# Kernel optimization log

Measured on AMD Instinct MI355X. Metric: run time of the kernel, lower is better.

## Reference

```python
import math
import jax, jax.numpy as jnp
import numpy as np

B, L, D, H = 4, 2048, 512, 8
DK = D // H  # d_keys = d_values = 64
KFAC = 3


def setup_inputs() -> dict:
    key = jax.random.key(0)
    ks = jax.random.split(key, 10)
    u_part = min(KFAC * int(math.ceil(math.log(L))), L)  # 24
    scale = 1.0 / math.sqrt(D)
    return {
        "queries": jax.random.normal(ks[0], (B, L, D), jnp.float32),
        "keys": jax.random.normal(ks[1], (B, L, D), jnp.float32),
        "values": jax.random.normal(ks[2], (B, L, D), jnp.float32),
        "index_sample": jax.random.randint(ks[3], (L, u_part), 0, L, jnp.int32),
        "Wq": jax.random.normal(ks[4], (D, D), jnp.float32) * scale,
        "bq": jnp.zeros((D,), jnp.float32),
        "Wk": jax.random.normal(ks[5], (D, D), jnp.float32) * scale,
        "bk": jnp.zeros((D,), jnp.float32),
        "Wv": jax.random.normal(ks[6], (D, D), jnp.float32) * scale,
        "bv": jnp.zeros((D,), jnp.float32),
        "Wo": jax.random.normal(ks[7], (D, D), jnp.float32) * scale,
        "bo": jnp.zeros((D,), jnp.float32),
    }


def reference(queries, keys, values, index_sample, Wq, bq, Wk, bk, Wv, bv, Wo, bo):
    b, q_len, d_out = queries.shape
    k_len = keys.shape[1]
    # projections -> [B, H, L, DK]
    q = (queries @ Wq + bq).reshape(b, q_len, H, DK).transpose(0, 2, 1, 3)
    k = (keys @ Wk + bk).reshape(b, k_len, H, DK).transpose(0, 2, 1, 3)
    v = (values @ Wv + bv).reshape(b, k_len, H, DK).transpose(0, 2, 1, 3)

    n_top = min(KFAC * int(math.ceil(math.log(q_len))), q_len)  # u

    # --- _prob_qk: sampled QK scores to pick sparse queries ---
    # k_sample: [B, H, q_len, sample_k, DK]
    k_sample = k[:, :, index_sample, :]
    q_k_sample = jnp.einsum("bhld,bhlsd->bhls", q, k_sample)
    m = jnp.max(q_k_sample, axis=-1) - jnp.sum(q_k_sample, axis=-1) / k_len
    _, m_top = jax.lax.top_k(m, n_top)  # [B, H, u]

    q_reduce = jnp.take_along_axis(q, m_top[..., None], axis=2)  # [B, H, u, DK]
    scores_top = jnp.einsum("bhud,bhkd->bhuk", q_reduce, k) / math.sqrt(d_out)

    # --- masked (causal) branch: mask_flag=True ---
    causal = jnp.triu(jnp.ones((q_len, k_len), bool), 1)
    indicator = causal[m_top]  # [B, H, u, k_len]
    scores_top = jnp.where(indicator, -jnp.inf, scores_top)

    attn = jax.nn.softmax(scores_top, axis=-1)  # [B, H, u, k_len]
    context = jnp.cumsum(v, axis=2)  # default context for non-selected queries
    attn_values = jnp.einsum("bhuk,bhkd->bhud", attn, v)

    bidx = jnp.arange(b)[:, None, None]
    hidx = jnp.arange(H)[None, :, None]
    context = context.at[bidx, hidx, m_top].set(attn_values)

    # mix=False: transpose back to [B, L, H, DV] then merge heads
    context = context.transpose(0, 2, 1, 3).reshape(b, q_len, H * DK)
    out = context @ Wo + bo  # dropout_rate=0 / inference: identity
    return out
```

## Files before the change

### kernel.cpp

```cpp
#include <hip/hip_runtime.h>
#include <hip/hip_bf16.h>
#include <math.h>

#define Bq 4
#define Lq 2048
#define Dq 512
#define Hq 8
#define DKq 64
#define Uq 24
#define TSCAN 16
#define NTILE (Lq / TSCAN)
#define JCH 256
#define NCH (Lq / JCH)
#define TKCH 8
#define PAD 40

typedef unsigned short ushort_t;
typedef unsigned long long u64;
typedef __attribute__((ext_vector_type(8))) short bfrag8;
typedef __attribute__((ext_vector_type(4))) float facc4;

__device__ inline ushort_t bf16_rne(float f) {
  unsigned u = __float_as_uint(f);
  u += 0x7FFF + ((u >> 16) & 1);
  return (ushort_t)(u >> 16);
}
__device__ inline float bf16f(ushort_t h) {
  return __uint_as_float(((unsigned)h) << 16);
}
__device__ inline unsigned fkey(float f) {
  unsigned u = __float_as_uint(f);
  return (u & 0x80000000u) ? ~u : (u | 0x80000000u);
}

__global__ __launch_bounds__(256) void transpose_cast4(
    const float* __restrict__ W0, const float* __restrict__ W1,
    const float* __restrict__ W2, const float* __restrict__ W3,
    ushort_t* __restrict__ T0h, ushort_t* __restrict__ T0l,
    ushort_t* __restrict__ T1h, ushort_t* __restrict__ T1l,
    ushort_t* __restrict__ T2h, ushort_t* __restrict__ T3h) {
  __shared__ float tile[32][33];
  int z = blockIdx.z;
  const float* W = z == 0 ? W0 : (z == 1 ? W1 : (z == 2 ? W2 : W3));
  ushort_t* Th = z == 0 ? T0h : (z == 1 ? T1h : (z == 2 ? T2h : T3h));
  ushort_t* Tl = z == 0 ? T0l : (z == 1 ? T1l : nullptr);
  int k0 = blockIdx.x * 32, n0 = blockIdx.y * 32;
  int tx = threadIdx.x & 31, ty = threadIdx.x >> 5;
  for (int r = ty; r < 32; r += 8)
    tile[tx][r] = W[(size_t)(k0 + r) * 512 + n0 + tx];
  __syncthreads();
  for (int r = ty; r < 32; r += 8) {
    float v = tile[r][tx];
    ushort_t h = bf16_rne(v);
    Th[(size_t)(n0 + r) * 512 + k0 + tx] = h;
    if (Tl) Tl[(size_t)(n0 + r) * 512 + k0 + tx] = bf16_rne(v - bf16f(h));
  }
}

__global__ __launch_bounds__(256) void gemm_qkv(
    const float* __restrict__ Xq, const float* __restrict__ Xk,
    const float* __restrict__ Xv,
    const ushort_t* __restrict__ Wqh, const ushort_t* __restrict__ Wql,
    const ushort_t* __restrict__ Wkh, const ushort_t* __restrict__ Wkl,
    const ushort_t* __restrict__ Wvh,
    const float* __restrict__ bq, const float* __restrict__ bk,
    const float* __restrict__ bv,
    float* __restrict__ qo, float* __restrict__ ko, float* __restrict__ vo) {
  __shared__ ushort_t Ash[128][PAD], Asl[128][PAD];
  __shared__ ushort_t Bsh[128][PAD], Bsl[128][PAD];
  int which = blockIdx.z;
  const float* A = which == 0 ? Xq : (which == 1 ? Xk : Xv);
  const ushort_t* Bh = which == 0 ? Wqh : (which == 1 ? Wkh : Wvh);
  const ushort_t* Bl = which == 0 ? Wql : Wkl;
  const float* bias = which == 0 ? bq : (which == 1 ? bk : bv);
  float* C = which == 0 ? qo : (which == 1 ? ko : vo);
  const bool split = which < 2;

  int bm = blockIdx.x, bn = blockIdx.y;
  int tid = threadIdx.x;
  int wave = tid >> 6, lane = tid & 63;
  int wm = (wave & 1) * 64, wn = (wave >> 1) * 64;
  int quad = lane >> 4, lm = lane & 15;
  facc4 acc[4][4] = {};

  for (int k0 = 0; k0 < 512; k0 += 32) {
#pragma unroll
    for (int p = 0; p < 2; ++p) {
      int s = p * 256 + tid;
      int row = s >> 2, kq = (s & 3) * 8;
      const float* src = &A[(size_t)(bm * 128 + row) * 512 + k0 + kq];
      float4 x0 = *(const float4*)src;
      float4 x1 = *(const float4*)(src + 4);
      float xs[8] = {x0.x, x0.y, x0.z, x0.w, x1.x, x1.y, x1.z, x1.w};
      bfrag8 hv;
#pragma unroll
      for (int e = 0; e < 8; ++e) hv[e] = (short)bf16_rne(xs[e]);
      *(bfrag8*)&Ash[row][kq] = hv;
      if (split) {
        bfrag8 lv;
#pragma unroll
        for (int e = 0; e < 8; ++e)
          lv[e] = (short)bf16_rne(xs[e] - bf16f((ushort_t)hv[e]));
        *(bfrag8*)&Asl[row][kq] = lv;
      }
    }
#pragma unroll
    for (int p = 0; p < 2; ++p) {
      int s = p * 256 + tid;
      int row = s >> 2, kq = (s & 3) * 8;
      size_t g = (size_t)(bn * 128 + row) * 512 + k0 + kq;
      *(bfrag8*)&Bsh[row][kq] = *(const bfrag8*)&Bh[g];
      if (split) *(bfrag8*)&Bsl[row][kq] = *(const bfrag8*)&Bl[g];
    }
    __syncthreads();
    bfrag8 afh[4], afl[4], bfh[4], bfl[4];
#pragma unroll
    for (int mt = 0; mt < 4; ++mt) {
      afh[mt] = *(bfrag8*)&Ash[wm + mt * 16 + lm][quad * 8];
      if (split) afl[mt] = *(bfrag8*)&Asl[wm + mt * 16 + lm][quad * 8];
    }
#pragma unroll
    for (int nt = 0; nt < 4; ++nt) {
      bfh[nt] = *(bfrag8*)&Bsh[wn + nt * 16 + lm][quad * 8];
      if (split) bfl[nt] = *(bfrag8*)&Bsl[wn + nt * 16 + lm][quad * 8];
    }
#pragma unroll
    for (int mt = 0; mt < 4; ++mt)
#pragma unroll
      for (int nt = 0; nt < 4; ++nt) {
        facc4 a = acc[mt][nt];
        a = __builtin_amdgcn_mfma_f32_16x16x32_bf16(afh[mt], bfh[nt], a, 0, 0, 0);
        if (split) {
          a = __builtin_amdgcn_mfma_f32_16x16x32_bf16(afl[mt], bfh[nt], a, 0, 0, 0);
          a = __builtin_amdgcn_mfma_f32_16x16x32_bf16(afh[mt], bfl[nt], a, 0, 0, 0);
        }
        acc[mt][nt] = a;
      }
    __syncthreads();
  }
#pragma unroll
  for (int mt = 0; mt < 4; ++mt)
#pragma unroll
    for (int nt = 0; nt < 4; ++nt) {
      int col = bn * 128 + wn + nt * 16 + lm;
      float bv2 = bias[col];
#pragma unroll
      for (int r = 0; r < 4; ++r) {
        int row = bm * 128 + wm + mt * 16 + quad * 4 + r;
        C[(size_t)row * 512 + col] = acc[mt][nt][r] + bv2;
      }
    }
}

__global__ __launch_bounds__(256) void gemm_bf16(
    const ushort_t* __restrict__ A, const ushort_t* __restrict__ Bt,
    const float* __restrict__ bias, float* __restrict__ C) {
  __shared__ ushort_t As[128][PAD];
  __shared__ ushort_t Bs[128][PAD];
  int bm = blockIdx.x, bn = blockIdx.y;
  int tid = threadIdx.x;
  int wave = tid >> 6, lane = tid & 63;
  int wm = (wave & 1) * 64, wn = (wave >> 1) * 64;
  int quad = lane >> 4, lm = lane & 15;
  facc4 acc[4][4] = {};

  for (int k0 = 0; k0 < 512; k0 += 32) {
#pragma unroll
    for (int p = 0; p < 2; ++p) {
      int s = p * 256 + tid;
      int row = s >> 2, kq = (s & 3) * 8;
      *(bfrag8*)&As[row][kq] =
          *(const bfrag8*)&A[(size_t)(bm * 128 + row) * 512 + k0 + kq];
      *(bfrag8*)&Bs[row][kq] =
          *(const bfrag8*)&Bt[(size_t)(bn * 128 + row) * 512 + k0 + kq];
    }
    __syncthreads();
    bfrag8 af[4], bf[4];
#pragma unroll
    for (int mt = 0; mt < 4; ++mt)
      af[mt] = *(bfrag8*)&As[wm + mt * 16 + lm][quad * 8];
#pragma unroll
    for (int nt = 0; nt < 4; ++nt)
      bf[nt] = *(bfrag8*)&Bs[wn + nt * 16 + lm][quad * 8];
#pragma unroll
    for (int mt = 0; mt < 4; ++mt)
#pragma unroll
      for (int nt = 0; nt < 4; ++nt)
        acc[mt][nt] = __builtin_amdgcn_mfma_f32_16x16x32_bf16(
            af[mt], bf[nt], acc[mt][nt], 0, 0, 0);
    __syncthreads();
  }
#pragma unroll
  for (int mt = 0; mt < 4; ++mt)
#pragma unroll
    for (int nt = 0; nt < 4; ++nt) {
      int col = bn * 128 + wn + nt * 16 + lm;
      float bv = bias[col];
#pragma unroll
      for (int r = 0; r < 4; ++r) {
        int row = bm * 128 + wm + mt * 16 + quad * 4 + r;
        C[(size_t)row * 512 + col] = acc[mt][nt][r] + bv;
      }
    }
}

__global__ __launch_bounds__(256) void compute_m(
    const float* __restrict__ q, const float* __restrict__ k,
    const int* __restrict__ idxs, float* __restrict__ m) {
  int wave = threadIdx.x >> 6, lane = threadIdx.x & 63;
  int lq = lane >> 4, dq = lane & 15;
  int slot = (blockIdx.x * 4 + wave) * 4 + lq;
  int l = slot & (Lq - 1);
  int bh = slot >> 11;
  int h = bh & (Hq - 1), b = bh >> 3;
  float4 qv = *(const float4*)&q[((size_t)b * Lq + l) * Dq + h * DKq + dq * 4];
  const float* kb = &k[(size_t)b * Lq * Dq + h * DKq + dq * 4];
  const int* ib = &idxs[l * Uq];
  float mx = -INFINITY, sm = 0.f;
#pragma unroll
  for (int s = 0; s < Uq; ++s) {
    int j = ib[s];
    float4 kv = *(const float4*)&kb[(size_t)j * Dq];
    float p = qv.x * kv.x + qv.y * kv.y + qv.z * kv.z + qv.w * kv.w;
    p += __shfl_xor(p, 1, 64);
    p += __shfl_xor(p, 2, 64);
    p += __shfl_xor(p, 4, 64);
    p += __shfl_xor(p, 8, 64);
    mx = fmaxf(mx, p);
    sm += p;
  }
  if (dq == 0) m[slot] = mx - sm * (1.0f / Lq);
}

__device__ inline void bitonic256_desc(u64* s, int tid) {
  for (int k = 2; k <= 256; k <<= 1) {
    for (int j = k >> 1; j > 0; j >>= 1) {
      int p = tid ^ j;
      u64 mine = s[tid], other = s[p];
      u64 mx = mine > other ? mine : other;
      u64 mn = mine > other ? other : mine;
      bool dir = (tid & k) == 0;
      bool lower = tid < p;
      u64 res = dir ? (lower ? mx : mn) : (lower ? mn : mx);
      __syncthreads();
      s[tid] = res;
      __syncthreads();
    }
  }
}

__global__ __launch_bounds__(256) void topk_stage1(
    const float* __restrict__ m, u64* __restrict__ cand) {
  __shared__ u64 s[256];
  int bh = blockIdx.x >> 3;
  int ch = blockIdx.x & 7;
  int tid = threadIdx.x;
  int gidx = ch * 256 + tid;
  float v = m[(size_t)bh * Lq + gidx];
  s[tid] = ((u64)fkey(v) << 32) | (u64)(Lq - 1 - gidx);
  __syncthreads();
  bitonic256_desc(s, tid);
  if (tid < Uq) cand[((size_t)bh * TKCH + ch) * Uq + tid] = s[tid];
}

__global__ __launch_bounds__(256) void topk_stage2(
    const u64* __restrict__ cand, int* __restrict__ mtop) {
  __shared__ u64 s[256];
  int bh = blockIdx.x;
  int tid = threadIdx.x;
  s[tid] = (tid < TKCH * Uq) ? cand[(size_t)bh * TKCH * Uq + tid] : 0ull;
  __syncthreads();
  bitonic256_desc(s, tid);
  if (tid < Uq) mtop[bh * Uq + tid] = Lq - 1 - (int)(s[tid] & 0xFFFFFFFFull);
}

__global__ __launch_bounds__(256) void make_repl(
    const int* __restrict__ mtop, int* __restrict__ repl) {
  __shared__ int mt[Uq];
  int bh = blockIdx.x >> 3;
  int ch = blockIdx.x & 7;
  int tid = threadIdx.x;
  if (tid < Uq) mt[tid] = mtop[bh * Uq + tid];
  __syncthreads();
  int l = ch * 256 + tid;
  int u = -1;
#pragma unroll
  for (int s = 0; s < Uq; ++s)
    if (mt[s] == l) u = s;
  repl[(size_t)bh * Lq + l] = u;
}

#define JT 256
#define JS 64

__global__ __launch_bounds__(256) void scores_kernel(
    const float* __restrict__ q, const float* __restrict__ k,
    const int* __restrict__ mtop, float* __restrict__ scg) {
  __shared__ float qs[Uq][DKq + 1];
  __shared__ float ks[JS][DKq + 1];
  __shared__ int i0s[Uq];
  int bh = blockIdx.y;
  int jt = blockIdx.x;
  int h = bh & (Hq - 1);
  int b = bh >> 3;
  int tid = threadIdx.x;
  if (tid < Uq) i0s[tid] = mtop[bh * Uq + tid];
  __syncthreads();
  for (int s = tid; s < Uq * 16; s += 256) {
    int u = s >> 4, qd = (s & 15) * 4;
    float4 t = *(const float4*)&q[((size_t)b * Lq + i0s[u]) * Dq + h * DKq + qd];
    qs[u][qd] = t.x; qs[u][qd + 1] = t.y; qs[u][qd + 2] = t.z; qs[u][qd + 3] = t.w;
  }
  int jp = tid & 31;
  int ug = tid >> 5;
  const float scale = 0.044194173824159216f;
  for (int sub = 0; sub < JT / JS; ++sub) {
    int jbase = jt * JT + sub * JS;
    __syncthreads();
    for (int s = tid; s < JS * 16; s += 256) {
      int j = s >> 4, qd = (s & 15) * 4;
      float4 t = *(const float4*)&k[((size_t)b * Lq + jbase + j) * Dq + h * DKq + qd];
      ks[j][qd] = t.x; ks[j][qd + 1] = t.y; ks[j][qd + 2] = t.z; ks[j][qd + 3] = t.w;
    }
    __syncthreads();
    float acc[3][2] = {};
    int j0 = jp * 2, j1 = j0 + 1;
#pragma unroll 8
    for (int d = 0; d < DKq; ++d) {
      float k0 = ks[j0][d], k1 = ks[j1][d];
#pragma unroll
      for (int uu = 0; uu < 3; ++uu) {
        float qv = qs[ug * 3 + uu][d];
        acc[uu][0] += qv * k0;
        acc[uu][1] += qv * k1;
      }
    }
#pragma unroll
    for (int uu = 0; uu < 3; ++uu) {
      int u = ug * 3 + uu;
      scg[((size_t)(bh * Uq + u)) * Lq + jbase + j0] = acc[uu][0] * scale;
      scg[((size_t)(bh * Uq + u)) * Lq + jbase + j1] = acc[uu][1] * scale;
    }
  }
}

__global__ __launch_bounds__(256) void softmax_pv_partial(
    const float* __restrict__ scg, const float* __restrict__ v,
    const int* __restrict__ mtop, float* __restrict__ pmax,
    float* __restrict__ psum, float* __restrict__ pvp) {
  int blk = blockIdx.y;
  int jc = blockIdx.x;
  int bh = blk / Uq;
  int h = bh & (Hq - 1);
  int b = bh >> 3;
  int n = mtop[blk] + 1;
  int j0 = jc * JCH;
  if (j0 >= n) return;
  int cnt = min(JCH, n - j0);
  int tid = threadIdx.x, wave = tid >> 6, lane = tid & 63;
  __shared__ float es[JCH];
  __shared__ float red[4][DKq];
  __shared__ float rr[4];

  const float* row = &scg[(size_t)blk * Lq + j0];
  float mx = (tid < cnt) ? row[tid] : -INFINITY;
#pragma unroll
  for (int off = 32; off; off >>= 1) mx = fmaxf(mx, __shfl_xor(mx, off, 64));
  if (lane == 0) rr[wave] = mx;
  __syncthreads();
  mx = fmaxf(fmaxf(rr[0], rr[1]), fmaxf(rr[2], rr[3]));
  __syncthreads();

  float e = (tid < cnt) ? __expf(row[tid] - mx) : 0.f;
  es[tid] = e;
  float sm = e;
#pragma unroll
  for (int off = 32; off; off >>= 1) sm += __shfl_xor(sm, off, 64);
  if (lane == 0) rr[wave] = sm;
  __syncthreads();

  float acc = 0.f;
  const float* vb = &v[((size_t)b * Lq + j0) * Dq + h * DKq + lane];
  int jlo = wave * 64;
  int jhi = min(jlo + 64, cnt);
#pragma unroll 4
  for (int j = jlo; j < jhi; ++j) acc += es[j] * vb[(size_t)j * Dq];
  red[wave][lane] = acc;
  __syncthreads();
  if (wave == 0) {
    if (lane == 0) {
      pmax[blk * NCH + jc] = mx;
      psum[blk * NCH + jc] = rr[0] + rr[1] + rr[2] + rr[3];
    }
    pvp[((size_t)blk * NCH + jc) * DKq + lane] =
        red[0][lane] + red[1][lane] + red[2][lane] + red[3][lane];
  }
}

__global__ __launch_bounds__(256) void softmax_pv_combine(
    const float* __restrict__ pmax, const float* __restrict__ psum,
    const float* __restrict__ pvp, const int* __restrict__ mtop,
    float* __restrict__ attnv) {
  int blk = blockIdx.x * 4 + (threadIdx.x >> 6);
  int lane = threadIdx.x & 63;
  int n = mtop[blk] + 1;
  int nc = (n + JCH - 1) / JCH;
  float gmax = -INFINITY;
  for (int c = 0; c < nc; ++c) gmax = fmaxf(gmax, pmax[blk * NCH + c]);
  float tot = 0.f, acc = 0.f;
  for (int c = 0; c < nc; ++c) {
    float w = __expf(pmax[blk * NCH + c] - gmax);
    tot += psum[blk * NCH + c] * w;
    acc += pvp[((size_t)blk * NCH + c) * DKq + lane] * w;
  }
  attnv[(size_t)blk * DKq + lane] = acc / tot;
}

__global__ __launch_bounds__(128) void tile_sum(const float* __restrict__ v,
                                                float* __restrict__ tsum) {
  int blk = blockIdx.x;
  int tile = blk & (NTILE - 1);
  int b = blk >> 7;
  int d4 = threadIdx.x;
  float4 s = {0.f, 0.f, 0.f, 0.f};
  const float* base = &v[((size_t)b * Lq + tile * TSCAN) * Dq + d4 * 4];
#pragma unroll
  for (int r = 0; r < TSCAN; ++r) {
    float4 x = *(const float4*)&base[(size_t)r * Dq];
    s.x += x.x; s.y += x.y; s.z += x.z; s.w += x.w;
  }
  *(float4*)&tsum[((size_t)b * NTILE + tile) * Dq + d4 * 4] = s;
}

__global__ __launch_bounds__(128) void build_context(
    const float* __restrict__ v, const float* __restrict__ tsum,
    const int* __restrict__ repl, const float* __restrict__ attnv,
    ushort_t* __restrict__ ctxh) {
  int blk = blockIdx.x;
  int tile = blk & (NTILE - 1);
  int b = blk >> 7;
  int d4 = threadIdx.x;
  int h = d4 >> 4;
  float4 run = {0.f, 0.f, 0.f, 0.f};
  const float* tb = &tsum[(size_t)b * NTILE * Dq + d4 * 4];
  for (int i = 0; i < tile; ++i) {
    float4 t = *(const float4*)&tb[(size_t)i * Dq];
    run.x += t.x; run.y += t.y; run.z += t.z; run.w += t.w;
  }
  const int* replb = &repl[(size_t)(b * Hq + h) * Lq + tile * TSCAN];
  const float* vb = &v[((size_t)b * Lq + tile * TSCAN) * Dq + d4 * 4];
  ushort_t* cb = &ctxh[((size_t)b * Lq + tile * TSCAN) * Dq + d4 * 4];
  const float* ab = &attnv[(size_t)(b * Hq + h) * Uq * DKq + (d4 & 15) * 4];
#pragma unroll
  for (int r = 0; r < TSCAN; ++r) {
    float4 x = *(const float4*)&vb[(size_t)r * Dq];
    run.x += x.x; run.y += x.y; run.z += x.z; run.w += x.w;
    int u = replb[r];
    float4 val = run;
    if (u >= 0) val = *(const float4*)&ab[(size_t)u * DKq];
    ushort4 o = {bf16_rne(val.x), bf16_rne(val.y), bf16_rne(val.z),
                 bf16_rne(val.w)};
    *(ushort4*)&cb[(size_t)r * Dq] = o;
  }
}

extern "C" void kernel_launch(void* const* d_in, const int* in_sizes, int n_in,
                              void* d_out, int out_size, void* d_ws,
                              size_t ws_size, hipStream_t stream) {
  const float* queries = (const float*)d_in[0];
  const float* keys    = (const float*)d_in[1];
  const float* values  = (const float*)d_in[2];
  const int*   idxs    = (const int*)d_in[3];
  const float* Wq = (const float*)d_in[4];
  const float* bq = (const float*)d_in[5];
  const float* Wk = (const float*)d_in[6];
  const float* bk = (const float*)d_in[7];
  const float* Wv = (const float*)d_in[8];
  const float* bv = (const float*)d_in[9];
  const float* Wo = (const float*)d_in[10];
  const float* bo = (const float*)d_in[11];
  float* out = (float*)d_out;

  const size_t BLD = (size_t)Bq * Lq * Dq;
  char* w = (char*)d_ws;
  float* q    = (float*)w; w += BLD * 4;
  float* k    = (float*)w; w += BLD * 4;
  float* v    = (float*)w; w += BLD * 4;
  float* scg  = (float*)w; w += (size_t)Bq * Hq * Uq * Lq * 4;
  float* m    = (float*)w; w += (size_t)Bq * Hq * Lq * 4;
  float* attnv= (float*)w; w += (size_t)Bq * Hq * Uq * DKq * 4;
  float* tsum = (float*)w; w += (size_t)Bq * NTILE * Dq * 4;
  int* mtop   = (int*)w;   w += Bq * Hq * Uq * 4;
  int* repl   = (int*)w;   w += (size_t)Bq * Hq * Lq * 4;
  float* pmax = (float*)w; w += (size_t)Bq * Hq * Uq * NCH * 4;
  float* psum = (float*)w; w += (size_t)Bq * Hq * Uq * NCH * 4;
  float* pvp  = (float*)w; w += (size_t)Bq * Hq * Uq * NCH * DKq * 4;
  u64* cand   = (u64*)w;   w += (size_t)Bq * Hq * TKCH * Uq * 8;
  ushort_t* ctxh = (ushort_t*)w; w += BLD * 2;
  const size_t WSZ = 512 * 512;
  ushort_t* Wqh = (ushort_t*)w; w += WSZ * 2;
  ushort_t* Wql = (ushort_t*)w; w += WSZ * 2;
  ushort_t* Wkh = (ushort_t*)w; w += WSZ * 2;
  ushort_t* Wkl = (ushort_t*)w; w += WSZ * 2;
  ushort_t* Wvh = (ushort_t*)w; w += WSZ * 2;
  ushort_t* Woh = (ushort_t*)w; w += WSZ * 2;

  {
    dim3 tgrid(16, 16, 4);
    transpose_cast4<<<tgrid, 256, 0, stream>>>(Wq, Wk, Wv, Wo, Wqh, Wql, Wkh,
                                               Wkl, Wvh, Woh);
  }

  {
    dim3 ggrid(64, 4, 3);
    gemm_qkv<<<ggrid, 256, 0, stream>>>(queries, keys, values, Wqh, Wql, Wkh,
                                        Wkl, Wvh, bq, bk, bv, q, k, v);
  }

  compute_m<<<(Bq * Hq * Lq) / 16, 256, 0, stream>>>(q, k, idxs, m);
  topk_stage1<<<Bq * Hq * TKCH, 256, 0, stream>>>(m, cand);
  topk_stage2<<<Bq * Hq, 256, 0, stream>>>(cand, mtop);
  make_repl<<<Bq * Hq * 8, 256, 0, stream>>>(mtop, repl);

  {
    dim3 sgrid(Lq / JT, Bq * Hq);
    scores_kernel<<<sgrid, 256, 0, stream>>>(q, k, mtop, scg);
  }
  {
    dim3 pgrid(NCH, Bq * Hq * Uq);
    softmax_pv_partial<<<pgrid, 256, 0, stream>>>(scg, v, mtop, pmax, psum, pvp);
    softmax_pv_combine<<<Bq * Hq * Uq / 4, 256, 0, stream>>>(pmax, psum, pvp,
                                                             mtop, attnv);
  }

  tile_sum<<<Bq * NTILE, 128, 0, stream>>>(v, tsum);
  build_context<<<Bq * NTILE, 128, 0, stream>>>(v, tsum, repl, attnv, ctxh);

  {
    dim3 ggrid(64, 4);
    gemm_bf16<<<ggrid, 256, 0, stream>>>(ctxh, Woh, bo, out);
  }
}
```

Before: 302.4 us.

## Pre-cast activations to bf16 hi/lo and load GEMM tiles via global_load_lds

Adds separate cast kernels that split the fp32 query/key/value inputs into bf16 hi (and lo) arrays ahead of time, so the QKV GEMM no longer converts inside its main loop. Both GEMMs now stage A/B tiles with direct global-to-LDS 16-byte loads and drop the LDS row padding. This is meant to cut per-tile VALU conversion and register round-trips in the GEMM loops. In exchange it adds three extra kernel launches and an extra full read/write pass over the activations. Unpadded LDS rows may also cause bank conflicts on the fragment reads.

```diff
diff --git a/kernel.cpp b/kernel.cpp
--- a/kernel.cpp
+++ b/kernel.cpp
@@ -13,7 +13,6 @@
 #define JCH 256
 #define NCH (Lq / JCH)
 #define TKCH 8
-#define PAD 40
 
 typedef unsigned short ushort_t;
 typedef unsigned long long u64;
@@ -31,6 +30,35 @@
 __device__ inline unsigned fkey(float f) {
   unsigned u = __float_as_uint(f);
   return (u & 0x80000000u) ? ~u : (u | 0x80000000u);
+}
+__device__ __forceinline__ void gl2lds16(const void* g, void* l) {
+  __builtin_amdgcn_global_load_lds(
+      (const __attribute__((address_space(1))) unsigned*)g,
+      (__attribute__((address_space(3))) unsigned*)l, 16, 0, 0);
+}
+
+__global__ __launch_bounds__(256) void cast_hilo(
+    const float* __restrict__ x, ushort_t* __restrict__ hi,
+    ushort_t* __restrict__ lo, int n4) {
+  int t = blockIdx.x * 256 + threadIdx.x;
+  if (t >= n4) return;
+  float4 v = *(const float4*)&x[(size_t)t * 4];
+  ushort_t h0 = bf16_rne(v.x), h1 = bf16_rne(v.y), h2 = bf16_rne(v.z),
+           h3 = bf16_rne(v.w);
+  ushort4 hh = {h0, h1, h2, h3};
+  ushort4 ll = {bf16_rne(v.x - bf16f(h0)), bf16_rne(v.y - bf16f(h1)),
+                bf16_rne(v.z - bf16f(h2)), bf16_rne(v.w - bf16f(h3))};
+  *(ushort4*)&hi[(size_t)t * 4] = hh;
+  *(ushort4*)&lo[(size_t)t * 4] = ll;
+}
+
+__global__ __launch_bounds__(256) void cast_hi(
+    const float* __restrict__ x, ushort_t* __restrict__ hi, int n4) {
+  int t = blockIdx.x * 256 + threadIdx.x;
+  if (t >= n4) return;
+  float4 v = *(const float4*)&x[(size_t)t * 4];
+  ushort4 hh = {bf16_rne(v.x), bf16_rne(v.y), bf16_rne(v.z), bf16_rne(v.w)};
+  *(ushort4*)&hi[(size_t)t * 4] = hh;
 }
 
 __global__ __launch_bounds__(256) void transpose_cast4(
@@ -58,18 +86,20 @@
 }
 
 __global__ __launch_bounds__(256) void gemm_qkv(
-    const float* __restrict__ Xq, const float* __restrict__ Xk,
-    const float* __restrict__ Xv,
+    const ushort_t* __restrict__ Aqh, const ushort_t* __restrict__ Aql,
+    const ushort_t* __restrict__ Akh, const ushort_t* __restrict__ Akl,
+    const ushort_t* __restrict__ Avh,
     const ushort_t* __restrict__ Wqh, const ushort_t* __restrict__ Wql,
     const ushort_t* __restrict__ Wkh, const ushort_t* __restrict__ Wkl,
     const ushort_t* __restrict__ Wvh,
     const float* __restrict__ bq, const float* __restrict__ bk,
     const float* __restrict__ bv,
     float* __restrict__ qo, float* __restrict__ ko, float* __restrict__ vo) {
-  __shared__ ushort_t Ash[128][PAD], Asl[128][PAD];
-  __shared__ ushort_t Bsh[128][PAD], Bsl[128][PAD];
+  __shared__ ushort_t Ash[128][32], Asl[128][32];
+  __shared__ ushort_t Bsh[128][32], Bsl[128][32];
   int which = blockIdx.z;
-  const float* A = which == 0 ? Xq : (which == 1 ? Xk : Xv);
+  const ushort_t* Ah = which == 0 ? Aqh : (which == 1 ? Akh : Avh);
+  const ushort_t* Al = which == 0 ? Aql : Akl;
   const ushort_t* Bh = which == 0 ? Wqh : (which == 1 ? Wkh : Wvh);
   const ushort_t* Bl = which == 0 ? Wql : Wkl;
   const float* bias = which == 0 ? bq : (which == 1 ? bk : bv);
@@ -81,36 +111,21 @@
   int wave = tid >> 6, lane = tid & 63;
   int wm = (wave & 1) * 64, wn = (wave >> 1) * 64;
   int quad = lane >> 4, lm = lane & 15;
+  int srow = tid >> 2, skq = (tid & 3) * 8;
   facc4 acc[4][4] = {};
 
   for (int k0 = 0; k0 < 512; k0 += 32) {
 #pragma unroll
     for (int p = 0; p < 2; ++p) {
-      int s = p * 256 + tid;
-      int row = s >> 2, kq = (s & 3) * 8;
-      const float* src = &A[(size_t)(bm * 128 + row) * 512 + k0 + kq];
-      float4 x0 = *(const float4*)src;
-      float4 x1 = *(const float4*)(src + 4);
-      float xs[8] = {x0.x, x0.y, x0.z, x0.w, x1.x, x1.y, x1.z, x1.w};
-      bfrag8 hv;
-#pragma unroll
-      for (int e = 0; e < 8; ++e) hv[e] = (short)bf16_rne(xs[e]);
-      *(bfrag8*)&Ash[row][kq] = hv;
+      int row = srow + p * 64;
+      size_t ga = (size_t)(bm * 128 + row) * 512 + k0 + skq;
+      size_t gb = (size_t)(bn * 128 + row) * 512 + k0 + skq;
+      gl2lds16(&Ah[ga], &Ash[row][skq]);
+      gl2lds16(&Bh[gb], &Bsh[row][skq]);
       if (split) {
-        bfrag8 lv;
-#pragma unroll
-        for (int e = 0; e < 8; ++e)
-          lv[e] = (short)bf16_rne(xs[e] - bf16f((ushort_t)hv[e]));
-        *(bfrag8*)&Asl[row][kq] = lv;
+        gl2lds16(&Al[ga], &Asl[row][skq]);
+        gl2lds16(&Bl[gb], &Bsl[row][skq]);
       }
-    }
-#pragma unroll
-    for (int p = 0; p < 2; ++p) {
-      int s = p * 256 + tid;
-      int row = s >> 2, kq = (s & 3) * 8;
-      size_t g = (size_t)(bn * 128 + row) * 512 + k0 + kq;
-      *(bfrag8*)&Bsh[row][kq] = *(const bfrag8*)&Bh[g];
-      if (split) *(bfrag8*)&Bsl[row][kq] = *(const bfrag8*)&Bl[g];
     }
     __syncthreads();
     bfrag8 afh[4], afl[4], bfh[4], bfl[4];
@@ -155,24 +170,22 @@
 __global__ __launch_bounds__(256) void gemm_bf16(
     const ushort_t* __restrict__ A, const ushort_t* __restrict__ Bt,
     const float* __restrict__ bias, float* __restrict__ C) {
-  __shared__ ushort_t As[128][PAD];
-  __shared__ ushort_t Bs[128][PAD];
+  __shared__ ushort_t As[128][32];
+  __shared__ ushort_t Bs[128][32];
   int bm = blockIdx.x, bn = blockIdx.y;
   int tid = threadIdx.x;
   int wave = tid >> 6, lane = tid & 63;
   int wm = (wave & 1) * 64, wn = (wave >> 1) * 64;
   int quad = lane >> 4, lm = lane & 15;
+  int srow = tid >> 2, skq = (tid & 3) * 8;
   facc4 acc[4][4] = {};
 
   for (int k0 = 0; k0 < 512; k0 += 32) {
 #pragma unroll
     for (int p = 0; p < 2; ++p) {
-      int s = p * 256 + tid;
-      int row = s >> 2, kq = (s & 3) * 8;
-      *(bfrag8*)&As[row][kq] =
-          *(const bfrag8*)&A[(size_t)(bm * 128 + row) * 512 + k0 + kq];
-      *(bfrag8*)&Bs[row][kq] =
-          *(const bfrag8*)&Bt[(size_t)(bn * 128 + row) * 512 + k0 + kq];
+      int row = srow + p * 64;
+      gl2lds16(&A[(size_t)(bm * 128 + row) * 512 + k0 + skq], &As[row][skq]);
+      gl2lds16(&Bt[(size_t)(bn * 128 + row) * 512 + k0 + skq], &Bs[row][skq]);
     }
     __syncthreads();
     bfrag8 af[4], bf[4];
@@ -497,6 +510,11 @@
   float* pvp  = (float*)w; w += (size_t)Bq * Hq * Uq * NCH * DKq * 4;
   u64* cand   = (u64*)w;   w += (size_t)Bq * Hq * TKCH * Uq * 8;
   ushort_t* ctxh = (ushort_t*)w; w += BLD * 2;
+  ushort_t* Aqh = (ushort_t*)w; w += BLD * 2;
+  ushort_t* Aql = (ushort_t*)w; w += BLD * 2;
+  ushort_t* Akh = (ushort_t*)w; w += BLD * 2;
+  ushort_t* Akl = (ushort_t*)w; w += BLD * 2;
+  ushort_t* Avh = (ushort_t*)w; w += BLD * 2;
   const size_t WSZ = 512 * 512;
   ushort_t* Wqh = (ushort_t*)w; w += WSZ * 2;
   ushort_t* Wql = (ushort_t*)w; w += WSZ * 2;
@@ -511,10 +529,15 @@
                                                Wkl, Wvh, Woh);
   }
 
+  const int CAST_B = (int)(BLD / 4 / 256);
+  cast_hilo<<<CAST_B, 256, 0, stream>>>(queries, Aqh, Aql, (int)(BLD / 4));
+  cast_hilo<<<CAST_B, 256, 0, stream>>>(keys, Akh, Akl, (int)(BLD / 4));
+  cast_hi<<<CAST_B, 256, 0, stream>>>(values, Avh, (int)(BLD / 4));
+
   {
     dim3 ggrid(64, 4, 3);
-    gemm_qkv<<<ggrid, 256, 0, stream>>>(queries, keys, values, Wqh, Wql, Wkh,
-                                        Wkl, Wvh, bq, bk, bv, q, k, v);
+    gemm_qkv<<<ggrid, 256, 0, stream>>>(Aqh, Aql, Akh, Akl, Avh, Wqh, Wql,
+                                        Wkh, Wkl, Wvh, bq, bk, bv, q, k, v);
   }
 
   compute_m<<<(Bq * Hq * Lq) / 16, 256, 0, stream>>>(q, k, idxs, m);
```

New measurement: 299.7 us. About the same (-0.9%).
